# Optimization experiments

Hardware: AMD Instinct MI355X
Metric: run time of the kernel (lower is better)

## Reference

```python
import jax, jax.numpy as jnp
import numpy as np
import math

BH, L, D = 128, 1024, 64  # batch*heads, maxLen, head_dim
MASK_VALUE = -1000000.0


def setup_inputs() -> dict:
    key = jax.random.key(0)
    kq, kk, kv, kl = jax.random.split(key, 4)
    return {
        "queries": jax.random.normal(kq, (BH, L, D), dtype=jnp.float32),
        "keys": jax.random.normal(kk, (BH, L, D), dtype=jnp.float32),
        "values": jax.random.normal(kv, (BH, L, D), dtype=jnp.float32),
        "valid_lens": jax.random.randint(kl, (BH,), 0, L, dtype=jnp.int32),
    }


def reference(queries, keys, values, valid_lens):
    d = queries.shape[-1]
    # scores: [BH, Lq, Lk]
    scores = jnp.einsum("bqd,bkd->bqk", queries, keys) / math.sqrt(d)
    # key-padding mask: position k valid iff k < valid_len[b]
    mask = jnp.arange(scores.shape[-1])[None, None, :] < valid_lens[:, None, None]
    scores = jnp.where(mask, scores, MASK_VALUE)
    attn = jax.nn.softmax(scores, axis=-1)
    # dropout is identity at inference (Keras Dropout, training=False)
    return jnp.einsum("bqk,bkd->bqd", attn, values)
```

## Files before the change

### kernel.cpp

```cpp
#include <hip/hip_runtime.h>
#include <hip/hip_bf16.h>

#define BH 128
#define L 1024
#define D 64
#define MASK_VALUE -1000000.0f
#define KVBLK 64
#define M0 12.0f

typedef __attribute__((ext_vector_type(8))) __bf16 bf16x8;
typedef __attribute__((ext_vector_type(4))) float f32x4;
typedef __attribute__((ext_vector_type(4))) unsigned int u32x4;

__device__ __forceinline__ unsigned short f2bf(float f) {
    __bf16 h = (__bf16)f;
    return __builtin_bit_cast(unsigned short, h);
}

__device__ __forceinline__ unsigned cvt_pk(float lo, float hi) {
    unsigned r;
    asm("v_cvt_pk_bf16_f32 %0, %1, %2" : "=v"(r) : "v"(lo), "v"(hi));
    return r;
}

__device__ __forceinline__ float exp2_asm(float x) {
    float r; asm("v_exp_f32 %0, %1" : "=v"(r) : "v"(x)); return r;
}

__device__ __forceinline__ f32x4 mfma16(bf16x8 a, bf16x8 b, f32x4 c) {
    return __builtin_amdgcn_mfma_f32_16x16x32_bf16(a, b, c, 0, 0, 0);
}

__device__ __forceinline__ bf16x8 ldsfrag(const unsigned char* base, int row, int colbytes) {
    const u32x4* p = (const u32x4*)(base + row * 128 + (colbytes ^ ((row & 7) << 4)));
    return __builtin_bit_cast(bf16x8, *p);
}

__device__ __forceinline__ int sigma_k(int k) {
    return (k & 0x23) | ((k & 0x0C) << 1) | ((k & 0x10) >> 2);
}

__global__ __launch_bounds__(512)
void attn_kernel(const float* __restrict__ Q, const float* __restrict__ K,
                 const float* __restrict__ V, const int* __restrict__ vlen,
                 float* __restrict__ Out) {
    __shared__ __align__(16) unsigned char Kl[2][64 * 128];
    __shared__ __align__(16) unsigned char Vl[2][64 * 128];

    const int tid  = threadIdx.x;
    const int lane = tid & 63;
    const int wid  = tid >> 6;

    const int bid  = blockIdx.x;
    const int xcd  = bid & 7;
    const int grp  = bid >> 3;
    const int head = xcd * 16 + (grp & 15);
    const int qt   = grp >> 4;

    const int valid = vlen[head];
    const int nkt   = (valid == 0) ? (L / KVBLK) : ((valid + KVBLK - 1) >> 6);
    const float MASKV = (valid == 0) ? -M0 : MASK_VALUE;

    const float* Qh = Q + (size_t)head * L * D;
    const float* Kh = K + (size_t)head * L * D;
    const float* Vh = V + (size_t)head * L * D;
    float*       Oh = Out + (size_t)head * L * D;

    const int qrow0 = qt * 128 + wid * 16;
    const int q16   = lane & 15;
    const int hi    = lane >> 4;
    const int c8    = hi * 8;

    const float QSCALE = 0.125f * 1.44269504088896f;
    bf16x8 qf[2];
#pragma unroll
    for (int kk = 0; kk < 2; ++kk) {
        const float* qp = Qh + (qrow0 + q16) * D + kk * 32 + c8;
        f32x4 a = *(const f32x4*)qp;
        f32x4 b = *(const f32x4*)(qp + 4);
        u32x4 w;
        w[0] = cvt_pk(a[0] * QSCALE, a[1] * QSCALE);
        w[1] = cvt_pk(a[2] * QSCALE, a[3] * QSCALE);
        w[2] = cvt_pk(b[0] * QSCALE, b[1] * QSCALE);
        w[3] = cvt_pk(b[2] * QSCALE, b[3] * QSCALE);
        qf[kk] = __builtin_bit_cast(bf16x8, w);
    }

    const int skr = tid >> 3;
    const int skc = (tid & 7) * 8;
    const int svk2 = (tid & 31) * 2;
    const int svd4 = (tid >> 5) * 4;
    const int svcb = sigma_k(svk2) * 2;

    f32x4 rk0, rk1;
    f32x4 rva, rvb;

    auto load_regs = [&](int kt) {
        const float* kp = Kh + (size_t)(kt * KVBLK + skr) * D + skc;
        rk0 = *(const f32x4*)kp;
        rk1 = *(const f32x4*)(kp + 4);
        const float* vp = Vh + (size_t)(kt * KVBLK + svk2) * D + svd4;
        rva = *(const f32x4*)vp;
        rvb = *(const f32x4*)(vp + D);
    };

    auto write_lds = [&](int buf) {
        unsigned char* kb = Kl[buf];
        u32x4 w;
        w[0] = cvt_pk(rk0[0], rk0[1]);
        w[1] = cvt_pk(rk0[2], rk0[3]);
        w[2] = cvt_pk(rk1[0], rk1[1]);
        w[3] = cvt_pk(rk1[2], rk1[3]);
        *(u32x4*)(kb + skr * 128 + ((skc * 2) ^ ((skr & 7) << 4))) = w;
        unsigned char* vb = Vl[buf];
#pragma unroll
        for (int j = 0; j < 4; ++j) {
            int row = svd4 + j;
            *(unsigned*)(vb + row * 128 + (svcb ^ ((row & 7) << 4))) = cvt_pk(rva[j], rvb[j]);
        }
    };

    f32x4 o[4];
#pragma unroll
    for (int t = 0; t < 4; ++t) { o[t][0] = 0.f; o[t][1] = 0.f; o[t][2] = 0.f; o[t][3] = 0.f; }
    float l_part = 0.f;

    load_regs(0);
    write_lds(0);
    __syncthreads();

    for (int kt = 0; kt < nkt; ++kt) {
        const int  cur      = kt & 1;
        const bool has_next = (kt + 1 < nkt);
        if (has_next) load_regs(kt + 1);

        f32x4 s[4];
        __builtin_amdgcn_s_setprio(1);
#pragma unroll
        for (int st = 0; st < 4; ++st) {
            bf16x8 kf0 = ldsfrag(Kl[cur], st * 16 + q16, c8 * 2);
            bf16x8 kf1 = ldsfrag(Kl[cur], st * 16 + q16, (32 + c8) * 2);
            f32x4 acc; acc[0] = -M0; acc[1] = -M0; acc[2] = -M0; acc[3] = -M0;
            acc = mfma16(kf0, qf[0], acc);
            acc = mfma16(kf1, qf[1], acc);
            s[st] = acc;
        }
        __builtin_amdgcn_s_setprio(0);

        if ((kt + 1) * KVBLK > valid) {
            const int kb = kt * KVBLK + hi * 4;
#pragma unroll
            for (int st = 0; st < 4; ++st)
#pragma unroll
                for (int r = 0; r < 4; ++r)
                    if (kb + st * 16 + r >= valid) s[st][r] = MASKV;
        }

#pragma unroll
        for (int st = 0; st < 4; ++st)
#pragma unroll
            for (int r = 0; r < 4; ++r)
                s[st][r] = exp2_asm(s[st][r]);

        u32x4 pw0, pw1;
        pw0[0] = cvt_pk(s[0][0], s[0][1]); pw0[1] = cvt_pk(s[0][2], s[0][3]);
        pw0[2] = cvt_pk(s[1][0], s[1][1]); pw0[3] = cvt_pk(s[1][2], s[1][3]);
        pw1[0] = cvt_pk(s[2][0], s[2][1]); pw1[1] = cvt_pk(s[2][2], s[2][3]);
        pw1[2] = cvt_pk(s[3][0], s[3][1]); pw1[3] = cvt_pk(s[3][2], s[3][3]);
        bf16x8 pf0 = __builtin_bit_cast(bf16x8, pw0);
        bf16x8 pf1 = __builtin_bit_cast(bf16x8, pw1);

        __builtin_amdgcn_s_setprio(1);
#pragma unroll
        for (int t = 0; t < 4; ++t) {
            bf16x8 vf0 = ldsfrag(Vl[cur], t * 16 + q16, c8 * 2);
            bf16x8 vf1 = ldsfrag(Vl[cur], t * 16 + q16, (32 + c8) * 2);
            o[t] = mfma16(pf0, vf0, o[t]);
            o[t] = mfma16(pf1, vf1, o[t]);
        }
        __builtin_amdgcn_s_setprio(0);

        float u0 = (s[0][0] + s[0][1]) + (s[0][2] + s[0][3]);
        float u1 = (s[1][0] + s[1][1]) + (s[1][2] + s[1][3]);
        float u2 = (s[2][0] + s[2][1]) + (s[2][2] + s[2][3]);
        float u3 = (s[3][0] + s[3][1]) + (s[3][2] + s[3][3]);
        l_part += (u0 + u1) + (u2 + u3);

        if (has_next) write_lds((kt + 1) & 1);
        __syncthreads();
    }

    float lsum = l_part;
    lsum += __shfl_xor(lsum, 16);
    lsum += __shfl_xor(lsum, 32);
    float linv = 1.0f / lsum;
    float r0 = __shfl(linv, hi * 4 + 0);
    float r1 = __shfl(linv, hi * 4 + 1);
    float r2 = __shfl(linv, hi * 4 + 2);
    float r3 = __shfl(linv, hi * 4 + 3);
#pragma unroll
    for (int t = 0; t < 4; ++t) {
        const int d = t * 16 + q16;
        Oh[(size_t)(qrow0 + hi * 4 + 0) * D + d] = o[t][0] * r0;
        Oh[(size_t)(qrow0 + hi * 4 + 1) * D + d] = o[t][1] * r1;
        Oh[(size_t)(qrow0 + hi * 4 + 2) * D + d] = o[t][2] * r2;
        Oh[(size_t)(qrow0 + hi * 4 + 3) * D + d] = o[t][3] * r3;
    }
}

extern "C" void kernel_launch(void* const* d_in, const int* in_sizes, int n_in,
                              void* d_out, int out_size, void* d_ws, size_t ws_size,
                              hipStream_t stream) {
    const float* Q    = (const float*)d_in[0];
    const float* K    = (const float*)d_in[1];
    const float* V    = (const float*)d_in[2];
    const int*   vlen = (const int*)d_in[3];
    float*       Out  = (float*)d_out;

    dim3 grid(BH * (L / 128));
    attn_kernel<<<grid, 512, 0, stream>>>(Q, K, V, vlen, Out);
}
```

Measured before the change: 50.59 us.

## Sort heads by KV tile count and serpentine-schedule blocks across XCDs

Adds a small pre-kernel that ranks heads by the number of KV tiles they need (descending) and writes a permutation to workspace. The attention kernel then maps block IDs to heads through this permutation. Each XCD receives heads interleaved from the sorted order, and within an XCD work is assigned in a snake pattern. The goal is longest-job-first scheduling with per-XCD balance, reducing tail imbalance caused by the variable valid_lens. The cost is an extra kernel launch and a dependent global read per block.

```diff
diff --git a/kernel.cpp b/kernel.cpp
--- a/kernel.cpp
+++ b/kernel.cpp
@@ -40,10 +40,25 @@
     return (k & 0x23) | ((k & 0x0C) << 1) | ((k & 0x10) >> 2);
 }
 
+__device__ __forceinline__ int nkt_of(int valid) {
+    return (valid == 0) ? (L / KVBLK) : ((valid + KVBLK - 1) >> 6);
+}
+
+__global__ void sort_heads(const int* __restrict__ vlen, int* __restrict__ perm) {
+    const int j  = threadIdx.x;
+    const int nk = nkt_of(vlen[j]);
+    int r = 0;
+    for (int i = 0; i < BH; ++i) {
+        const int nki = nkt_of(vlen[i]);
+        if (nki > nk || (nki == nk && i < j)) ++r;
+    }
+    perm[r] = j;
+}
+
 __global__ __launch_bounds__(512)
 void attn_kernel(const float* __restrict__ Q, const float* __restrict__ K,
                  const float* __restrict__ V, const int* __restrict__ vlen,
-                 float* __restrict__ Out) {
+                 const int* __restrict__ perm, float* __restrict__ Out) {
     __shared__ __align__(16) unsigned char Kl[2][64 * 128];
     __shared__ __align__(16) unsigned char Vl[2][64 * 128];
 
@@ -53,12 +68,16 @@
 
     const int bid  = blockIdx.x;
     const int xcd  = bid & 7;
-    const int grp  = bid >> 3;
-    const int head = xcd * 16 + (grp & 15);
-    const int qt   = grp >> 4;
+    const int slot = bid >> 3;
+    const int c    = slot & 31;
+    const int rr   = slot >> 5;
+    const int idx  = (rr & 1) ? (rr * 32 + 31 - c) : (rr * 32 + c);
+    const int l    = idx >> 3;
+    const int qt   = idx & 7;
+    const int head = perm[(l << 3) | xcd];
 
     const int valid = vlen[head];
-    const int nkt   = (valid == 0) ? (L / KVBLK) : ((valid + KVBLK - 1) >> 6);
+    const int nkt   = nkt_of(valid);
     const float MASKV = (valid == 0) ? -M0 : MASK_VALUE;
 
     const float* Qh = Q + (size_t)head * L * D;
@@ -216,7 +235,9 @@
     const float* V    = (const float*)d_in[2];
     const int*   vlen = (const int*)d_in[3];
     float*       Out  = (float*)d_out;
-
+    int*         perm = (int*)d_ws;
+
+    sort_heads<<<1, 128, 0, stream>>>(vlen, perm);
     dim3 grid(BH * (L / 128));
-    attn_kernel<<<grid, 512, 0, stream>>>(Q, K, V, vlen, Out);
-}
+    attn_kernel<<<grid, 512, 0, stream>>>(Q, K, V, vlen, perm, Out);
+}
```

Measured after the change: 43.95 us (median of 2 runs). 13.1% less time.
